# Kernel tuning notes

Hardware: AMD Instinct MI355X
Metric: run time of the kernel (lower is better)

## Reference

```python
import jax, jax.numpy as jnp
import numpy as np

N_NODES = 50000
N_EDGES = 500000
IN_DIM = 32
HID = 64
NUM_GRAPHS = 64


def _inv(d):
    # 1/d with inf -> 0, as in PyG HypergraphConv
    return jnp.where(d > 0, 1.0 / d, 0.0)


def hypergraph_conv(xh, row0, row1, W, b, n_hnodes, n_hedges):
    """PyG HypergraphConv (heads=1, no attention, unit hyperedge weights).
    xh: (n_hnodes, din) hyper-node features; row0: hyper-node ids, row1: hyperedge ids.
    Index n_hnodes / n_hedges is a padding slot for masked-out incidences.
    """
    xw = xh @ W                                   # (n_hnodes, dout) Theta
    xw = jnp.concatenate([xw, jnp.zeros((1, xw.shape[1]), xw.dtype)], axis=0)
    ones = jnp.ones(row0.shape[0], xw.dtype)
    D = _inv(jax.ops.segment_sum(ones, row0, num_segments=n_hnodes + 1))  # node degree^-1
    B = _inv(jax.ops.segment_sum(ones, row1, num_segments=n_hedges + 1))  # edge size^-1
    # node -> hyperedge aggregation, scaled by B
    he = jax.ops.segment_sum(xw[row0], row1, num_segments=n_hedges + 1) * B[:, None]
    # hyperedge -> node aggregation, scaled by D
    out = jax.ops.segment_sum(he[row1], row0, num_segments=n_hnodes + 1) * D[:, None]
    return out[:n_hnodes] + b


def setup_inputs() -> dict:
    key = jax.random.key(0)
    ks = jax.random.split(key, 12)
    x = jax.random.normal(ks[0], (N_NODES, 16), jnp.float32)
    edge_attr = jax.random.normal(ks[1], (N_EDGES, IN_DIM), jnp.float32)
    edge_index = jax.random.randint(ks[2], (2, N_EDGES), 0, N_NODES, dtype=jnp.int64)
    batch = jnp.sort(jax.random.randint(ks[3], (N_NODES,), 0, NUM_GRAPHS, dtype=jnp.int64))
    node_imp = jax.random.uniform(ks[4], (N_NODES,), jnp.float32)
    s = 0.05
    W0 = jax.random.normal(ks[5], (IN_DIM, HID), jnp.float32) * s
    b0 = jax.random.normal(ks[6], (HID,), jnp.float32) * s
    W1 = jax.random.normal(ks[7], (HID, HID), jnp.float32) * s
    b1 = jax.random.normal(ks[8], (HID,), jnp.float32) * s
    W2 = jax.random.normal(ks[9], (HID, HID), jnp.float32) * s
    b2 = jax.random.normal(ks[10], (HID,), jnp.float32) * s
    return {"x": x, "edge_attr": edge_attr, "edge_index": edge_index, "batch": batch,
            "node_imp": node_imp, "W0": W0, "b0": b0, "W1": W1, "b1": b1,
            "W2": W2, "b2": b2, "num_graphs": NUM_GRAPHS}


def reference(x, edge_attr, edge_index, batch, node_imp, W0, b0, W1, b1, W2, b2, num_graphs):
    N = x.shape[0]
    E = edge_index.shape[1]
    edge_imp = jnp.minimum(node_imp[edge_index[0]], node_imp[edge_index[1]])
    # --- Dual Hypergraph Transform (get_DHT) ---
    row0 = jnp.repeat(jnp.arange(E), 2)            # hyper-node = original edge id
    row1 = edge_index.T.reshape(-1)                # hyperedge  = original node id
    deg = jax.ops.segment_sum(jnp.ones(2 * E, jnp.float32), row1, num_segments=N)
    keep = deg[row1] != 1.0                        # drop incidences of degree-1 hyperedges
    row0 = jnp.where(keep, row0, E)                # redirect dropped entries to padding slot
    row1 = jnp.where(keep, row1, N + E)
    # self-loops: hyperedge ids N..N+E-1 (equivalent to torch's max_edge+1.., since
    # unused hyperedge slots receive nothing and B^-1 there is 0)
    row0 = jnp.concatenate([row0, jnp.arange(E)])
    row1 = jnp.concatenate([row1, N + jnp.arange(E)])
    edge_batch = batch[edge_index[0]]              # == hyperedge_index[1].reshape(-1,2)[:,0]
    # --- conv stack (dropout in eval mode = identity) ---
    h = edge_attr * edge_imp[:, None]
    xs = []
    for (W, b) in ((W0, b0), (W1, b1), (W2, b2)):
        h = jax.nn.relu(hypergraph_conv(h, row0, row1, W, b, E, N + E))
        h = h * edge_imp[:, None]
        xs.append(h)
    gh = jnp.concatenate(
        [jax.ops.segment_sum(h_i, edge_batch, num_segments=num_graphs) for h_i in xs], axis=1)
    return gh
```

## Files before the change

### kernel.cpp

```cpp
#include <hip/hip_runtime.h>
#include <hip/hip_bf16.h>
#include <cstdint>
#include <cstddef>

typedef unsigned short u16;
typedef unsigned int   u32;
typedef short bf16x8 __attribute__((ext_vector_type(8)));
typedef float f32x4  __attribute__((ext_vector_type(4)));

struct __align__(16) ERec { u32 uv; float iu, iv, ie; };
struct __align__(8) NRec { float dinv; float imp; };

#define NCOPY 8

__device__ __forceinline__ float bf2f(u16 v){ return __uint_as_float(((u32)v)<<16); }
__device__ __forceinline__ u16 f2bf(float f){
  u32 x = __float_as_uint(f);
  return (u16)((x + 0x7FFFu + ((x>>16)&1u)) >> 16);
}
__device__ __forceinline__ void atomAddF(float* p, float v){ unsafeAtomicAdd(p, v); }
__device__ __forceinline__ float rlanef(float v, int q){
  return __int_as_float(__builtin_amdgcn_readlane(__float_as_int(v), q));
}

__global__ void kzero(int* p, int n){
  int i = blockIdx.x*blockDim.x + threadIdx.x;
  if(i < n) p[i] = 0;
}

__global__ void kdeg2p(const int* __restrict__ ei0, const int* __restrict__ ei1,
                       int* __restrict__ deg0c, int* __restrict__ deg1c,
                       int* __restrict__ r0, int* __restrict__ r1,
                       int N, int E){
  int e = blockIdx.x*blockDim.x + threadIdx.x;
  if(e >= E) return;
  const int c = blockIdx.x & (NCOPY-1);
  r0[e] = atomicAdd(&deg0c[c*N + ei0[e]], 1);
  r1[e] = atomicAdd(&deg1c[c*N + ei1[e]], 1);
}

__global__ void kreduce(const int* __restrict__ deg0c, const int* __restrict__ deg1c,
                        int* __restrict__ deg0, int* __restrict__ deg1,
                        int* __restrict__ cb0, int* __restrict__ cb1, int N){
  int i = blockIdx.x*blockDim.x + threadIdx.x;
  if(i < N){
    int s = 0;
    #pragma unroll
    for(int c = 0; c < NCOPY; c++){ int t = deg0c[c*N+i]; cb0[c*N+i] = s; s += t; }
    deg0[i] = s;
  } else if(i < 2*N){
    int j = i - N;
    int s = 0;
    #pragma unroll
    for(int c = 0; c < NCOPY; c++){ int t = deg1c[c*N+j]; cb1[c*N+j] = s; s += t; }
    deg1[j] = s;
  }
}

__global__ __launch_bounds__(256) void ktilesum(const int* __restrict__ deg0,
                                                const int* __restrict__ deg1,
                                                int* __restrict__ tsum,
                                                int N, int nt){
  __shared__ int sh[256];
  const int b = blockIdx.x;
  const int* deg = (b < nt) ? deg0 : deg1;
  const int tile = (b < nt) ? b : b - nt;
  const int t = threadIdx.x;
  const int i = tile*256 + t;
  sh[t] = (i < N) ? deg[i] : 0;
  __syncthreads();
  for(int s = 128; s > 0; s >>= 1){
    if(t < s) sh[t] += sh[t+s];
    __syncthreads();
  }
  if(t == 0) tsum[b] = sh[0];
}
__global__ __launch_bounds__(256) void kmid(int* __restrict__ tsum,
                                            int* __restrict__ off0,
                                            int* __restrict__ off1,
                                            int N, int nt){
  __shared__ int sh[256];
  const int b = blockIdx.x;
  int* ts = tsum + b*nt;
  const int t = threadIdx.x;
  sh[t] = (t < nt) ? ts[t] : 0;
  __syncthreads();
  for(int s = 1; s < 256; s <<= 1){
    int x = (t >= s) ? sh[t-s] : 0;
    __syncthreads();
    sh[t] += x;
    __syncthreads();
  }
  if(t < nt) ts[t] = (t == 0) ? 0 : sh[t-1];
  if(t == 255){ int* off = b ? off1 : off0; off[N] = sh[255]; }
}
__global__ __launch_bounds__(256) void kapply(const int* __restrict__ deg0,
                                              const int* __restrict__ deg1,
                                              const int* __restrict__ tsum,
                                              int* __restrict__ off0,
                                              int* __restrict__ off1,
                                              const float* __restrict__ nimp,
                                              NRec* __restrict__ nrec,
                                              int N, int nt){
  __shared__ int sh[256];
  const int b = blockIdx.x;
  const int* deg = (b < nt) ? deg0 : deg1;
  int*       off = (b < nt) ? off0 : off1;
  const int tile = (b < nt) ? b : b - nt;
  const int base = tsum[b];
  const int t = threadIdx.x;
  const int i = tile*256 + t;
  sh[t] = (i < N) ? deg[i] : 0;
  __syncthreads();
  for(int s = 1; s < 256; s <<= 1){
    int x = (t >= s) ? sh[t-s] : 0;
    __syncthreads();
    sh[t] += x;
    __syncthreads();
  }
  if(i < N){
    off[i] = base + ((t == 0) ? 0 : sh[t-1]);
    if(b < nt){
      int d = deg0[i] + deg1[i];
      NRec r;
      r.dinv = (d > 1) ? (1.f/(float)d) : 0.f;
      r.imp  = nimp[i];
      nrec[i] = r;
    }
  }
}

__global__ void kpermv(const int* __restrict__ ei0, const int* __restrict__ ei1,
                       const NRec* __restrict__ nrec,
                       const int* __restrict__ off0, const int* __restrict__ off1,
                       const int* __restrict__ cb0, const int* __restrict__ cb1,
                       const int* __restrict__ r0, const int* __restrict__ r1,
                       ERec* __restrict__ rec,
                       int* __restrict__ iperm, float* __restrict__ impO,
                       int* __restrict__ list1, int E, int N){
  int e = blockIdx.x*blockDim.x + threadIdx.x;
  if(e >= E) return;
  const int c = blockIdx.x & (NCOPY-1);
  int u = ei0[e], v = ei1[e];
  NRec ru = nrec[u];
  NRec rv = nrec[v];
  int pos = off0[u] + cb0[c*N+u] + r0[e];
  float ie = fminf(ru.imp, rv.imp);
  ERec r;
  r.uv = (u32)u | ((u32)v << 16);
  r.iu = ru.dinv; r.iv = rv.dinv; r.ie = ie;
  rec[pos]  = r;
  iperm[e]  = pos;
  impO[e]   = ie;
  int p1 = off1[v] + cb1[c*N+v] + r1[e];
  list1[p1] = pos;
}

__global__ void kprepw(const float* __restrict__ W0, u16* __restrict__ wf0,
                       const float* __restrict__ W1, u16* __restrict__ wf1,
                       const float* __restrict__ W2, u16* __restrict__ wf2){
  const int b = blockIdx.x;
  const float* W; u16* wf; int NC, sbase;
  if(b == 0){ W = W0; wf = wf0; NC = 1; sbase = 0; }
  else if(b <= 2){ W = W1; wf = wf1; NC = 2; sbase = (b-1)*256; }
  else { W = W2; wf = wf2; NC = 2; sbase = (b-3)*256; }
  int s = sbase + threadIdx.x;
  if(s >= 4*NC*64) return;
  int lane = s & 63;
  int c    = (s >> 6) % NC;
  int tt   = s / (NC*64);
  int n  = tt*16 + (lane & 15);
  int k0 = c*32 + (lane >> 4)*8;
  #pragma unroll
  for(int j = 0; j < 8; j++)
    wf[(size_t)s*8 + j] = f2bf(W[(size_t)(k0 + j)*64 + n]);
}

__global__ __launch_bounds__(256) void kgemm0(const float* __restrict__ srcf,
                                              u16* __restrict__ buf,
                                              const u16* __restrict__ wf,
                                              const float* __restrict__ impO,
                                              const int* __restrict__ iperm,
                                              int E){
  const int t    = threadIdx.x;
  const int wv   = t >> 6;
  const int lane = t & 63;
  const int quad = lane >> 4;
  const int l15  = lane & 15;
  const int row0 = blockIdx.x*64 + wv*16;
  if(row0 >= E) return;

  bf16x8 bfr[4];
  #pragma unroll
  for(int i = 0; i < 4; i++)
    bfr[i] = *(const bf16x8*)(wf + ((size_t)i*64 + lane)*8);

  const int myrow = row0 + l15;
  const float* s = srcf + (size_t)myrow*32 + quad*8;
  const float sc = impO[myrow];
  const int ip = iperm[myrow];
  f32x4 v0 = *(const f32x4*)s;
  f32x4 v1 = *(const f32x4*)(s+4);
  bf16x8 afr;
  afr[0]=(short)f2bf(v0.x*sc); afr[1]=(short)f2bf(v0.y*sc);
  afr[2]=(short)f2bf(v0.z*sc); afr[3]=(short)f2bf(v0.w*sc);
  afr[4]=(short)f2bf(v1.x*sc); afr[5]=(short)f2bf(v1.y*sc);
  afr[6]=(short)f2bf(v1.z*sc); afr[7]=(short)f2bf(v1.w*sc);

  int dr[4];
  #pragma unroll
  for(int r = 0; r < 4; r++) dr[r] = __shfl(ip, quad*4 + r);

  #pragma unroll
  for(int tt = 0; tt < 4; tt++){
    f32x4 a = {0.f,0.f,0.f,0.f};
    a = __builtin_amdgcn_mfma_f32_16x16x32_bf16(afr, bfr[tt], a, 0, 0, 0);
    const int n = tt*16 + l15;
    #pragma unroll
    for(int r = 0; r < 4; r++)
      buf[(size_t)dr[r]*64 + n] = f2bf(a[r]);
  }
}

__global__ __launch_bounds__(256) void kagg(const u16* __restrict__ buf,
                                            const int* __restrict__ off0,
                                            const int* __restrict__ off1,
                                            const int* __restrict__ list1,
                                            u16* __restrict__ heb, int N){
  const int t = threadIdx.x, wv = t >> 6, lane = t & 63;
  const int n = blockIdx.x*4 + wv;
  if(n >= N) return;
  const int rsub = lane >> 3, cb = lane & 7;
  float acc[8];
  #pragma unroll
  for(int k = 0; k < 8; k++) acc[k] = 0.f;

  auto accum = [&](uint4 x){
    acc[0] += bf2f((u16)x.x); acc[1] += bf2f((u16)(x.x>>16));
    acc[2] += bf2f((u16)x.y); acc[3] += bf2f((u16)(x.y>>16));
    acc[4] += bf2f((u16)x.z); acc[5] += bf2f((u16)(x.z>>16));
    acc[6] += bf2f((u16)x.w); acc[7] += bf2f((u16)(x.w>>16));
  };
  const uint4 zero4 = {0,0,0,0};

  {
    const int s0 = off0[n], d0 = off0[n+1] - s0;
    const u16* base = buf + (size_t)s0*64;
    int j = 0;
    for(; j + 8 <= d0; j += 8)
      accum(*(const uint4*)(base + (size_t)(j+rsub)*64 + cb*8));
    if(j < d0)
      accum((rsub < d0-j) ? *(const uint4*)(base + (size_t)(j+rsub)*64 + cb*8) : zero4);
  }
  {
    const int s1 = off1[n], d1 = off1[n+1] - s1;
    int j = 0;
    for(; j + 8 <= d1; j += 8){
      int e = list1[s1 + j + rsub];
      accum(*(const uint4*)(buf + (size_t)e*64 + cb*8));
    }
    if(j < d1){
      uint4 x = zero4;
      if(rsub < d1-j){
        int e = list1[s1 + j + rsub];
        x = *(const uint4*)(buf + (size_t)e*64 + cb*8);
      }
      accum(x);
    }
  }
  #pragma unroll
  for(int m = 8; m <= 32; m <<= 1)
    #pragma unroll
    for(int k = 0; k < 8; k++) acc[k] += __shfl_xor(acc[k], m);
  if(rsub == 0){
    u32 o[4];
    #pragma unroll
    for(int k = 0; k < 4; k++)
      o[k] = (u32)f2bf(acc[2*k]) | ((u32)f2bf(acc[2*k+1]) << 16);
    *(uint4*)(heb + (size_t)n*64 + cb*8) = make_uint4(o[0],o[1],o[2],o[3]);
  }
}

template<bool DO_GEMM>
__global__ __launch_bounds__(256, 3) void kfused(u16* __restrict__ buf,
                                                 const u16* __restrict__ heb,
                                                 const f32x4* __restrict__ rec4,
                                                 const int* __restrict__ batch,
                                                 const float* __restrict__ bias,
                                                 const u16* __restrict__ wf,
                                                 float* __restrict__ ghL,
                                                 int E){
  constexpr int HTSZ = DO_GEMM ? 4*16*72 : 4;
  __shared__ __align__(16) u16 hT[HTSZ];
  const int t = threadIdx.x, wv = t >> 6, lane = t & 63;
  const int quad = lane >> 4, l15 = lane & 15;
  const float bd = bias[lane];

  bf16x8 bfr[8];
  if(DO_GEMM){
    #pragma unroll
    for(int i = 0; i < 8; i++)
      bfr[i] = *(const bf16x8*)(wf + ((size_t)i*64 + lane)*8);
  }

  float pool = 0.f;
  int cur_g = -1;
  const int base = __builtin_amdgcn_readfirstlane((int)(blockIdx.x*256) + wv*64);
  u16* hTw = DO_GEMM ? &hT[wv*1152] : &hT[0];

  u32 uvp = 0; f32x4 cf = {0.f,0.f,0.f,0.f}; int bt = 0;
  if(base < E){
    f32x4 w0 = rec4[(size_t)(base+l15)];
    uvp = __float_as_uint(w0.x);
    const float iu = w0.y, iv = w0.z;
    const float rc = (iu > 0.f && iv > 0.f) ? (1.f/3.f)
                   : ((iu > 0.f || iv > 0.f) ? 0.5f : 1.f);
    cf.x = rc; cf.y = iu*rc; cf.z = iv*rc; cf.w = w0.w;
    bt  = batch[uvp & 0xffffu];
  }

  #pragma unroll
  for(int it = 0; it < 4; it++){
    const int r0 = base + it*16;
    if(r0 < E){
      u16 bv[16], hu[16], hv[16];
      const u16* bufr = buf + (size_t)r0*64;
      #pragma unroll
      for(int q = 0; q < 16; q++){
        const u32 uv = (u32)__builtin_amdgcn_readlane((int)uvp, q);
        hv[q] = heb[(size_t)(uv >> 16)*64 + lane];
        hu[q] = heb[(size_t)(uv & 0xffffu)*64 + lane];
        bv[q] = bufr[q*64 + lane];
      }
      u32 uvpN = uvp; f32x4 cfN = cf; int btN = bt;
      if(it < 3){
        const int r1 = r0 + 16;
        if(r1 < E){
          f32x4 w0 = rec4[(size_t)(r1+l15)];
          uvpN = __float_as_uint(w0.x);
          const float iu = w0.y, iv = w0.z;
          const float rc = (iu > 0.f && iv > 0.f) ? (1.f/3.f)
                         : ((iu > 0.f || iv > 0.f) ? 0.5f : 1.f);
          cfN.x = rc; cfN.y = iu*rc; cfN.z = iv*rc; cfN.w = w0.w;
          btN  = batch[uvpN & 0xffffu];
        }
      }
      const int bFirst = __builtin_amdgcn_readlane(bt, 0);
      const int bLast  = __builtin_amdgcn_readlane(bt, 15);
      if(bFirst != cur_g){
        if(cur_g >= 0) atomAddF(&ghL[cur_g*192 + lane], pool);
        pool = 0.f; cur_g = bFirst;
      }
      if(bFirst == bLast){
        #pragma unroll
        for(int q = 0; q < 16; q++){
          const float rc   = rlanef(cf.x, q);
          const float iurc = rlanef(cf.y, q);
          const float ivrc = rlanef(cf.z, q);
          const float ie   = rlanef(cf.w, q);
          float o = fmaxf(fmaf(bf2f(bv[q]), rc,
                          fmaf(bf2f(hu[q]), iurc,
                          fmaf(bf2f(hv[q]), ivrc, bd))), 0.f) * ie;
          pool += o;
          if(DO_GEMM) hTw[q*72 + lane] = f2bf(o);
        }
      } else {
        #pragma unroll
        for(int q = 0; q < 16; q++){
          const float rc   = rlanef(cf.x, q);
          const float iurc = rlanef(cf.y, q);
          const float ivrc = rlanef(cf.z, q);
          const float ie   = rlanef(cf.w, q);
          const int   bq   = __builtin_amdgcn_readlane(bt, q);
          float o = fmaxf(fmaf(bf2f(bv[q]), rc,
                          fmaf(bf2f(hu[q]), iurc,
                          fmaf(bf2f(hv[q]), ivrc, bd))), 0.f) * ie;
          if(bq != cur_g){
            if(cur_g >= 0) atomAddF(&ghL[cur_g*192 + lane], pool);
            pool = 0.f; cur_g = bq;
          }
          pool += o;
          if(DO_GEMM) hTw[q*72 + lane] = f2bf(o);
        }
      }
      if(DO_GEMM){
        bf16x8 afr0 = *(const bf16x8*)&hTw[l15*72 + quad*8];
        bf16x8 afr1 = *(const bf16x8*)&hTw[l15*72 + 32 + quad*8];
        #pragma unroll
        for(int tt = 0; tt < 4; tt++){
          f32x4 a = {0.f,0.f,0.f,0.f};
          a = __builtin_amdgcn_mfma_f32_16x16x32_bf16(afr0, bfr[tt*2+0], a, 0, 0, 0);
          a = __builtin_amdgcn_mfma_f32_16x16x32_bf16(afr1, bfr[tt*2+1], a, 0, 0, 0);
          const int n = tt*16 + l15;
          #pragma unroll
          for(int r = 0; r < 4; r++)
            buf[(size_t)(r0 + quad*4 + r)*64 + n] = f2bf(a[r]);
        }
      }
      uvp = uvpN; cf = cfN; bt = btN;
    }
  }
  if(cur_g >= 0) atomAddF(&ghL[cur_g*192 + lane], pool);
}

__global__ void kfinal(const float* __restrict__ gh, float* __restrict__ out, int n){
  int i = blockIdx.x*blockDim.x + threadIdx.x;
  if(i < n) out[i] = gh[i];
}

extern "C" void kernel_launch(void* const* d_in, const int* in_sizes, int n_in,
                              void* d_out, int out_size, void* d_ws, size_t ws_size,
                              hipStream_t stream) {
  const float* edge_attr = (const float*)d_in[1];
  const int*   ei        = (const int*)d_in[2];
  const int*   batch     = (const int*)d_in[3];
  const float* nimp      = (const float*)d_in[4];
  const float* Ws[3] = { (const float*)d_in[5], (const float*)d_in[7], (const float*)d_in[9] };
  const float* bs[3] = { (const float*)d_in[6], (const float*)d_in[8], (const float*)d_in[10] };

  const int E = in_sizes[1] / 32;
  const int N = in_sizes[4];
  const int* ei0 = ei;
  const int* ei1 = ei + E;

  char* p = (char*)d_ws;
  auto carve = [&](size_t bytes)->char*{
    char* r = p; p += (bytes + 255) & ~(size_t)255; return r;
  };
  const int nt = (N + 255)/256;
  int*   deg0c = (int*)  carve((size_t)2*NCOPY*N*4);
  int*   deg1c = deg0c + NCOPY*N;
  int*   cb0   = (int*)  carve((size_t)2*NCOPY*N*4);
  int*   cb1   = cb0 + NCOPY*N;
  int*   r0    = (int*)  carve((size_t)2*E*4);
  int*   r1    = r0 + E;
  int*   deg0  = (int*)  carve((size_t)2*N*4);
  int*   deg1  = deg0 + N;
  NRec*  nrec  = (NRec*) carve((size_t)N*sizeof(NRec));
  int*   off0  = (int*)  carve((size_t)(N+1)*4);
  int*   off1  = (int*)  carve((size_t)(N+1)*4);
  int*   tsum  = (int*)  carve((size_t)2*nt*4);
  int*   iperm = (int*)  carve((size_t)E*4);
  float* impO  = (float*)carve((size_t)E*4);
  int*   list1 = (int*)  carve((size_t)E*4);
  ERec*  rec   = (ERec*) carve((size_t)E*sizeof(ERec));
  u16*   heb   = (u16*)  carve((size_t)N*64*2);
  u16*   buf   = (u16*)  carve((size_t)E*64*2);
  float* gh    = (float*)carve((size_t)64*192*4);
  u16*   wfs[3];
  for(int l = 0; l < 3; l++) wfs[l] = (u16*)carve((size_t)4096*2);

  kzero<<<(2*NCOPY*N+255)/256, 256, 0, stream>>>(deg0c, 2*NCOPY*N);
  kzero<<<(12288+255)/256, 256, 0, stream>>>((int*)gh, 12288);
  kdeg2p<<<(E+255)/256, 256, 0, stream>>>(ei0, ei1, deg0c, deg1c, r0, r1, N, E);
  kreduce<<<(2*N+255)/256, 256, 0, stream>>>(deg0c, deg1c, deg0, deg1, cb0, cb1, N);
  ktilesum<<<2*nt, 256, 0, stream>>>(deg0, deg1, tsum, N, nt);
  kmid<<<2, 256, 0, stream>>>(tsum, off0, off1, N, nt);
  kapply<<<2*nt, 256, 0, stream>>>(deg0, deg1, tsum, off0, off1, nimp, nrec, N, nt);
  kpermv<<<(E+255)/256, 256, 0, stream>>>(ei0, ei1, nrec, off0, off1, cb0, cb1,
                                          r0, r1, rec, iperm, impO, list1, E, N);
  kprepw<<<5, 256, 0, stream>>>(Ws[0], wfs[0], Ws[1], wfs[1], Ws[2], wfs[2]);

  const int nbG = (E + 63)/64;
  const int nbA = (N + 3)/4;
  const int nbF = (E + 255)/256;

  kgemm0<<<nbG, 256, 0, stream>>>(edge_attr, buf, wfs[0], impO, iperm, E);
  kagg<<<nbA, 256, 0, stream>>>(buf, off0, off1, list1, heb, N);
  kfused<true ><<<nbF, 256, 0, stream>>>(buf, heb, (const f32x4*)rec, batch, bs[0], wfs[1], gh + 0*64, E);
  kagg<<<nbA, 256, 0, stream>>>(buf, off0, off1, list1, heb, N);
  kfused<true ><<<nbF, 256, 0, stream>>>(buf, heb, (const f32x4*)rec, batch, bs[1], wfs[2], gh + 1*64, E);
  kagg<<<nbA, 256, 0, stream>>>(buf, off0, off1, list1, heb, N);
  kfused<false><<<nbF, 256, 0, stream>>>(buf, heb, (const f32x4*)rec, batch, bs[2], nullptr, gh + 2*64, E);
  kfinal<<<(12288+255)/256, 256, 0, stream>>>(gh, (float*)d_out, 12288);
}
```

Baseline: 401.1 us.

## Aggregate layer-0 inputs before projection to halve first-layer gather width

Layer 0 now permutes and scales the raw 32-wide edge features into a bf16 buffer, aggregates those 32-wide rows per node, and only then applies W0. This works because the linear transform commutes with the aggregation. A new fused kernel computes the layer-0 combination, GEMM, bias, ReLU, pooling and the layer-1 GEMM in one pass. The goal is to halve gather traffic in the first aggregation and to drop the scatter-write GEMM kernel. The cost is an extra prep kernel, extra buffers, and a wider per-wave fused kernel with more registers.

```diff
diff --git a/kernel.cpp b/kernel.cpp
--- a/kernel.cpp
+++ b/kernel.cpp
@@ -135,8 +135,7 @@
                        const int* __restrict__ off0, const int* __restrict__ off1,
                        const int* __restrict__ cb0, const int* __restrict__ cb1,
                        const int* __restrict__ r0, const int* __restrict__ r1,
-                       ERec* __restrict__ rec,
-                       int* __restrict__ iperm, float* __restrict__ impO,
+                       ERec* __restrict__ rec, int* __restrict__ orig,
                        int* __restrict__ list1, int E, int N){
   int e = blockIdx.x*blockDim.x + threadIdx.x;
   if(e >= E) return;
@@ -150,10 +149,29 @@
   r.uv = (u32)u | ((u32)v << 16);
   r.iu = ru.dinv; r.iv = rv.dinv; r.ie = ie;
   rec[pos]  = r;
-  iperm[e]  = pos;
-  impO[e]   = ie;
+  orig[pos] = e;
   int p1 = off1[v] + cb1[c*N+v] + r1[e];
   list1[p1] = pos;
+}
+
+__global__ __launch_bounds__(256) void kprep0(const float* __restrict__ ea,
+                                              const int* __restrict__ orig,
+                                              const float* __restrict__ recf,
+                                              u16* __restrict__ h0, int E){
+  int idx = blockIdx.x*256 + threadIdx.x;
+  int row = idx >> 2;
+  int c   = (idx & 3)*8;
+  if(row >= E) return;
+  int oe = orig[row];
+  float ie = recf[(size_t)row*4 + 3];
+  const float* s = ea + (size_t)oe*32 + c;
+  f32x4 v0 = *(const f32x4*)s;
+  f32x4 v1 = *(const f32x4*)(s+4);
+  u32 o0 = (u32)f2bf(v0.x*ie) | ((u32)f2bf(v0.y*ie) << 16);
+  u32 o1 = (u32)f2bf(v0.z*ie) | ((u32)f2bf(v0.w*ie) << 16);
+  u32 o2 = (u32)f2bf(v1.x*ie) | ((u32)f2bf(v1.y*ie) << 16);
+  u32 o3 = (u32)f2bf(v1.z*ie) | ((u32)f2bf(v1.w*ie) << 16);
+  *(uint4*)(h0 + (size_t)row*32 + c) = make_uint4(o0,o1,o2,o3);
 }
 
 __global__ void kprepw(const float* __restrict__ W0, u16* __restrict__ wf0,
@@ -176,52 +194,7 @@
     wf[(size_t)s*8 + j] = f2bf(W[(size_t)(k0 + j)*64 + n]);
 }
 
-__global__ __launch_bounds__(256) void kgemm0(const float* __restrict__ srcf,
-                                              u16* __restrict__ buf,
-                                              const u16* __restrict__ wf,
-                                              const float* __restrict__ impO,
-                                              const int* __restrict__ iperm,
-                                              int E){
-  const int t    = threadIdx.x;
-  const int wv   = t >> 6;
-  const int lane = t & 63;
-  const int quad = lane >> 4;
-  const int l15  = lane & 15;
-  const int row0 = blockIdx.x*64 + wv*16;
-  if(row0 >= E) return;
-
-  bf16x8 bfr[4];
-  #pragma unroll
-  for(int i = 0; i < 4; i++)
-    bfr[i] = *(const bf16x8*)(wf + ((size_t)i*64 + lane)*8);
-
-  const int myrow = row0 + l15;
-  const float* s = srcf + (size_t)myrow*32 + quad*8;
-  const float sc = impO[myrow];
-  const int ip = iperm[myrow];
-  f32x4 v0 = *(const f32x4*)s;
-  f32x4 v1 = *(const f32x4*)(s+4);
-  bf16x8 afr;
-  afr[0]=(short)f2bf(v0.x*sc); afr[1]=(short)f2bf(v0.y*sc);
-  afr[2]=(short)f2bf(v0.z*sc); afr[3]=(short)f2bf(v0.w*sc);
-  afr[4]=(short)f2bf(v1.x*sc); afr[5]=(short)f2bf(v1.y*sc);
-  afr[6]=(short)f2bf(v1.z*sc); afr[7]=(short)f2bf(v1.w*sc);
-
-  int dr[4];
-  #pragma unroll
-  for(int r = 0; r < 4; r++) dr[r] = __shfl(ip, quad*4 + r);
-
-  #pragma unroll
-  for(int tt = 0; tt < 4; tt++){
-    f32x4 a = {0.f,0.f,0.f,0.f};
-    a = __builtin_amdgcn_mfma_f32_16x16x32_bf16(afr, bfr[tt], a, 0, 0, 0);
-    const int n = tt*16 + l15;
-    #pragma unroll
-    for(int r = 0; r < 4; r++)
-      buf[(size_t)dr[r]*64 + n] = f2bf(a[r]);
-  }
-}
-
+template<int DIM>
 __global__ __launch_bounds__(256) void kagg(const u16* __restrict__ buf,
                                             const int* __restrict__ off0,
                                             const int* __restrict__ off1,
@@ -230,7 +203,9 @@
   const int t = threadIdx.x, wv = t >> 6, lane = t & 63;
   const int n = blockIdx.x*4 + wv;
   if(n >= N) return;
-  const int rsub = lane >> 3, cb = lane & 7;
+  constexpr int CB = DIM/8;
+  constexpr int RS = 64/CB;
+  const int rsub = lane / CB, cb = lane % CB;
   float acc[8];
   #pragma unroll
   for(int k = 0; k < 8; k++) acc[k] = 0.f;
@@ -245,31 +220,31 @@
 
   {
     const int s0 = off0[n], d0 = off0[n+1] - s0;
-    const u16* base = buf + (size_t)s0*64;
+    const u16* base = buf + (size_t)s0*DIM;
     int j = 0;
-    for(; j + 8 <= d0; j += 8)
-      accum(*(const uint4*)(base + (size_t)(j+rsub)*64 + cb*8));
+    for(; j + RS <= d0; j += RS)
+      accum(*(const uint4*)(base + (size_t)(j+rsub)*DIM + cb*8));
     if(j < d0)
-      accum((rsub < d0-j) ? *(const uint4*)(base + (size_t)(j+rsub)*64 + cb*8) : zero4);
+      accum((rsub < d0-j) ? *(const uint4*)(base + (size_t)(j+rsub)*DIM + cb*8) : zero4);
   }
   {
     const int s1 = off1[n], d1 = off1[n+1] - s1;
     int j = 0;
-    for(; j + 8 <= d1; j += 8){
+    for(; j + RS <= d1; j += RS){
       int e = list1[s1 + j + rsub];
-      accum(*(const uint4*)(buf + (size_t)e*64 + cb*8));
+      accum(*(const uint4*)(buf + (size_t)e*DIM + cb*8));
     }
     if(j < d1){
       uint4 x = zero4;
       if(rsub < d1-j){
         int e = list1[s1 + j + rsub];
-        x = *(const uint4*)(buf + (size_t)e*64 + cb*8);
+        x = *(const uint4*)(buf + (size_t)e*DIM + cb*8);
       }
       accum(x);
     }
   }
   #pragma unroll
-  for(int m = 8; m <= 32; m <<= 1)
+  for(int m = CB; m <= 32; m <<= 1)
     #pragma unroll
     for(int k = 0; k < 8; k++) acc[k] += __shfl_xor(acc[k], m);
   if(rsub == 0){
@@ -277,8 +252,164 @@
     #pragma unroll
     for(int k = 0; k < 4; k++)
       o[k] = (u32)f2bf(acc[2*k]) | ((u32)f2bf(acc[2*k+1]) << 16);
-    *(uint4*)(heb + (size_t)n*64 + cb*8) = make_uint4(o[0],o[1],o[2],o[3]);
-  }
+    *(uint4*)(heb + (size_t)n*DIM + cb*8) = make_uint4(o[0],o[1],o[2],o[3]);
+  }
+}
+
+__global__ __launch_bounds__(256, 3) void kfusedR1(const u16* __restrict__ h0,
+                                                   const u16* __restrict__ agg0,
+                                                   u16* __restrict__ buf,
+                                                   const f32x4* __restrict__ rec4,
+                                                   const int* __restrict__ batch,
+                                                   const float* __restrict__ bias0,
+                                                   const u16* __restrict__ wf0,
+                                                   const u16* __restrict__ wf1,
+                                                   float* __restrict__ gh0,
+                                                   int E){
+  __shared__ __align__(16) u16 hT[4*16*72];
+  __shared__ float ies[4][16];
+  const int t = threadIdx.x, wv = t >> 6, lane = t & 63;
+  const int quad = lane >> 4, l15 = lane & 15;
+  const int c32  = lane & 31;
+  u16* hTw = &hT[wv*1152];
+
+  float bd4[4];
+  #pragma unroll
+  for(int tt = 0; tt < 4; tt++) bd4[tt] = bias0[tt*16 + l15];
+
+  bf16x8 b0fr[4];
+  #pragma unroll
+  for(int i = 0; i < 4; i++)
+    b0fr[i] = *(const bf16x8*)(wf0 + ((size_t)i*64 + lane)*8);
+  bf16x8 b1fr[8];
+  #pragma unroll
+  for(int i = 0; i < 8; i++)
+    b1fr[i] = *(const bf16x8*)(wf1 + ((size_t)i*64 + lane)*8);
+
+  float pool[4] = {0.f,0.f,0.f,0.f};
+  int cur_g = -1;
+  const int base = __builtin_amdgcn_readfirstlane((int)(blockIdx.x*256) + wv*64);
+
+  auto flushPool = [&](){
+    #pragma unroll
+    for(int tt = 0; tt < 4; tt++){
+      float s = pool[tt];
+      s += __shfl_xor(s, 16);
+      s += __shfl_xor(s, 32);
+      if(quad == 0) atomAddF(&gh0[cur_g*192 + tt*16 + l15], s);
+      pool[tt] = 0.f;
+    }
+  };
+
+  u32 uvp = 0; f32x4 cf = {0.f,0.f,0.f,0.f}; int bt = 0;
+  if(base < E){
+    f32x4 w0 = rec4[(size_t)(base+l15)];
+    uvp = __float_as_uint(w0.x);
+    const float iu = w0.y, iv = w0.z;
+    const float rc = (iu > 0.f && iv > 0.f) ? (1.f/3.f)
+                   : ((iu > 0.f || iv > 0.f) ? 0.5f : 1.f);
+    cf.x = rc; cf.y = iu*rc; cf.z = iv*rc; cf.w = w0.w;
+    bt  = batch[uvp & 0xffffu];
+  }
+
+  #pragma unroll 1
+  for(int it = 0; it < 4; it++){
+    const int r0 = base + it*16;
+    if(r0 < E){
+      u16 zb[16], hu[16], hv[16];
+      const u16* h0r = h0 + (size_t)r0*32;
+      #pragma unroll
+      for(int q = 0; q < 16; q++){
+        const u32 uv = (u32)__builtin_amdgcn_readlane((int)uvp, q);
+        hv[q] = agg0[(size_t)(uv >> 16)*32 + c32];
+        hu[q] = agg0[(size_t)(uv & 0xffffu)*32 + c32];
+        zb[q] = h0r[q*32 + c32];
+      }
+      u32 uvpN = uvp; f32x4 cfN = cf; int btN = bt;
+      if(it < 3){
+        const int r1 = r0 + 16;
+        if(r1 < E){
+          f32x4 w0 = rec4[(size_t)(r1+l15)];
+          uvpN = __float_as_uint(w0.x);
+          const float iu = w0.y, iv = w0.z;
+          const float rc = (iu > 0.f && iv > 0.f) ? (1.f/3.f)
+                         : ((iu > 0.f || iv > 0.f) ? 0.5f : 1.f);
+          cfN.x = rc; cfN.y = iu*rc; cfN.z = iv*rc; cfN.w = w0.w;
+          btN  = batch[uvpN & 0xffffu];
+        }
+      }
+      if(lane < 16) ies[wv][lane] = cf.w;
+      #pragma unroll
+      for(int q = 0; q < 16; q++){
+        const float rc   = rlanef(cf.x, q);
+        const float iurc = rlanef(cf.y, q);
+        const float ivrc = rlanef(cf.z, q);
+        float z = fmaf(bf2f(zb[q]), rc,
+                  fmaf(bf2f(hu[q]), iurc, bf2f(hv[q])*ivrc));
+        if(lane < 32) hTw[q*72 + c32] = f2bf(z);
+      }
+      bf16x8 za = *(const bf16x8*)&hTw[l15*72 + quad*8];
+      f32x4 a0_[4];
+      #pragma unroll
+      for(int tt = 0; tt < 4; tt++){
+        f32x4 a = {0.f,0.f,0.f,0.f};
+        a = __builtin_amdgcn_mfma_f32_16x16x32_bf16(za, b0fr[tt], a, 0, 0, 0);
+        a0_[tt] = a;
+      }
+      float ier[4];
+      #pragma unroll
+      for(int r = 0; r < 4; r++) ier[r] = ies[wv][quad*4 + r];
+      float o[4][4];
+      #pragma unroll
+      for(int tt = 0; tt < 4; tt++)
+        #pragma unroll
+        for(int r = 0; r < 4; r++)
+          o[tt][r] = fmaxf(a0_[tt][r] + bd4[tt], 0.f) * ier[r];
+      const int bFirst = __builtin_amdgcn_readlane(bt, 0);
+      const int bLast  = __builtin_amdgcn_readlane(bt, 15);
+      if(bFirst == bLast){
+        if(bFirst != cur_g){
+          if(cur_g >= 0) flushPool();
+          cur_g = bFirst;
+        }
+        #pragma unroll
+        for(int tt = 0; tt < 4; tt++)
+          pool[tt] += (o[tt][0] + o[tt][1]) + (o[tt][2] + o[tt][3]);
+      } else {
+        #pragma unroll
+        for(int rr = 0; rr < 16; rr++){
+          const int bq = __builtin_amdgcn_readlane(bt, rr);
+          if(bq != cur_g){
+            if(cur_g >= 0) flushPool();
+            cur_g = bq;
+          }
+          if((rr >> 2) == quad){
+            #pragma unroll
+            for(int tt = 0; tt < 4; tt++) pool[tt] += o[tt][rr & 3];
+          }
+        }
+      }
+      #pragma unroll
+      for(int tt = 0; tt < 4; tt++)
+        #pragma unroll
+        for(int r = 0; r < 4; r++)
+          hTw[(quad*4 + r)*72 + tt*16 + l15] = f2bf(o[tt][r]);
+      bf16x8 afr0 = *(const bf16x8*)&hTw[l15*72 + quad*8];
+      bf16x8 afr1 = *(const bf16x8*)&hTw[l15*72 + 32 + quad*8];
+      #pragma unroll
+      for(int tt = 0; tt < 4; tt++){
+        f32x4 a = {0.f,0.f,0.f,0.f};
+        a = __builtin_amdgcn_mfma_f32_16x16x32_bf16(afr0, b1fr[tt*2+0], a, 0, 0, 0);
+        a = __builtin_amdgcn_mfma_f32_16x16x32_bf16(afr1, b1fr[tt*2+1], a, 0, 0, 0);
+        const int n = tt*16 + l15;
+        #pragma unroll
+        for(int r = 0; r < 4; r++)
+          buf[(size_t)(r0 + quad*4 + r)*64 + n] = f2bf(a[r]);
+      }
+      uvp = uvpN; cf = cfN; bt = btN;
+    }
+  }
+  if(cur_g >= 0) flushPool();
 }
 
 template<bool DO_GEMM>
@@ -440,10 +571,11 @@
   int*   off0  = (int*)  carve((size_t)(N+1)*4);
   int*   off1  = (int*)  carve((size_t)(N+1)*4);
   int*   tsum  = (int*)  carve((size_t)2*nt*4);
-  int*   iperm = (int*)  carve((size_t)E*4);
-  float* impO  = (float*)carve((size_t)E*4);
+  int*   orig  = (int*)  carve((size_t)E*4);
   int*   list1 = (int*)  carve((size_t)E*4);
   ERec*  rec   = (ERec*) carve((size_t)E*sizeof(ERec));
+  u16*   h0    = (u16*)  carve((size_t)E*32*2);
+  u16*   agg0  = (u16*)  carve((size_t)N*32*2);
   u16*   heb   = (u16*)  carve((size_t)N*64*2);
   u16*   buf   = (u16*)  carve((size_t)E*64*2);
   float* gh    = (float*)carve((size_t)64*192*4);
@@ -458,19 +590,19 @@
   kmid<<<2, 256, 0, stream>>>(tsum, off0, off1, N, nt);
   kapply<<<2*nt, 256, 0, stream>>>(deg0, deg1, tsum, off0, off1, nimp, nrec, N, nt);
   kpermv<<<(E+255)/256, 256, 0, stream>>>(ei0, ei1, nrec, off0, off1, cb0, cb1,
-                                          r0, r1, rec, iperm, impO, list1, E, N);
+                                          r0, r1, rec, orig, list1, E, N);
+  kprep0<<<((E*4)+255)/256, 256, 0, stream>>>(edge_attr, orig, (const float*)rec, h0, E);
   kprepw<<<5, 256, 0, stream>>>(Ws[0], wfs[0], Ws[1], wfs[1], Ws[2], wfs[2]);
 
-  const int nbG = (E + 63)/64;
   const int nbA = (N + 3)/4;
   const int nbF = (E + 255)/256;
 
-  kgemm0<<<nbG, 256, 0, stream>>>(edge_attr, buf, wfs[0], impO, iperm, E);
-  kagg<<<nbA, 256, 0, stream>>>(buf, off0, off1, list1, heb, N);
-  kfused<true ><<<nbF, 256, 0, stream>>>(buf, heb, (const f32x4*)rec, batch, bs[0], wfs[1], gh + 0*64, E);
-  kagg<<<nbA, 256, 0, stream>>>(buf, off0, off1, list1, heb, N);
+  kagg<32><<<nbA, 256, 0, stream>>>(h0, off0, off1, list1, agg0, N);
+  kfusedR1<<<nbF, 256, 0, stream>>>(h0, agg0, buf, (const f32x4*)rec, batch,
+                                    bs[0], wfs[0], wfs[1], gh + 0*64, E);
+  kagg<64><<<nbA, 256, 0, stream>>>(buf, off0, off1, list1, heb, N);
   kfused<true ><<<nbF, 256, 0, stream>>>(buf, heb, (const f32x4*)rec, batch, bs[1], wfs[2], gh + 1*64, E);
-  kagg<<<nbA, 256, 0, stream>>>(buf, off0, off1, list1, heb, N);
+  kagg<64><<<nbA, 256, 0, stream>>>(buf, off0, off1, list1, heb, N);
   kfused<false><<<nbF, 256, 0, stream>>>(buf, heb, (const f32x4*)rec, batch, bs[2], nullptr, gh + 2*64, E);
   kfinal<<<(12288+255)/256, 256, 0, stream>>>(gh, (float*)d_out, 12288);
 }
```

New measurement: 389.2 us. 1.03x faster.
